# Performance work log

Measured on AMD Instinct MI355X. Metric: run time of the kernel, lower is better.

## Reference

```python
import jax, jax.numpy as jnp
import numpy as np

NP, NM = 50, 32          # pathways, misc tokens
T = NP + NM              # 82 total tokens
D = 24                   # token_dim for latent_dim=2048: (2048//82)//4*4
H, DH, FF = 4, 6, 96     # heads, head_dim, ffn dim (4*D)
B = 8192
EPS = 1e-5


def _ln(x, g, b):
    m = x.mean(-1, keepdims=True)
    v = ((x - m) ** 2).mean(-1, keepdims=True)
    return (x - m) / jnp.sqrt(v + EPS) * g + b


def _adapter(x, w1, b1, g1, bb1, w2, b2, g2, bb2, w3, b3):
    # Linear -> LN -> GELU -> (Dropout eval) -> Linear -> LN -> GELU -> Linear
    h = jax.nn.gelu(_ln(x @ w1.T + b1, g1, bb1), approximate=False)
    h = jax.nn.gelu(_ln(h @ w2.T + b2, g2, bb2), approximate=False)
    return h @ w3.T + b3


def _enc_layer(x, wqkv, bqkv, wo, bo, lg1, lb1, fw1, fb1, fw2, fb2, lg2, lb2):
    # post-norm TransformerEncoderLayer (PyTorch defaults: relu FFN, batch_first)
    Bx, Tx, Dx = x.shape
    qkv = x @ wqkv.T + bqkv                       # [B,T,3D]
    q, k, v = jnp.split(qkv, 3, axis=-1)
    sh = lambda a: a.reshape(Bx, Tx, H, DH).transpose(0, 2, 1, 3)
    q, k, v = sh(q), sh(k), sh(v)
    att = jax.nn.softmax(jnp.einsum('bhqd,bhkd->bhqk', q, k) / jnp.sqrt(jnp.float32(DH)), axis=-1)
    o = jnp.einsum('bhqk,bhkd->bhqd', att, v).transpose(0, 2, 1, 3).reshape(Bx, Tx, Dx)
    o = o @ wo.T + bo
    x = _ln(x + o, lg1, lb1)
    f = jax.nn.relu(x @ fw1.T + fb1) @ fw2.T + fb2
    return _ln(x + f, lg2, lb2)


def setup_inputs() -> dict:
    key = jax.random.key(0)
    ks = iter(jax.random.split(key, 40))
    r = lambda *s: jax.random.normal(next(ks), s, dtype=jnp.float32) * 0.02
    inp = {
        'gene': jax.random.normal(next(ks), (B, 5000), dtype=jnp.float32),
        'protein': jax.random.normal(next(ks), (B, 226), dtype=jnp.float32),
        'pathway_tokens': jax.random.normal(next(ks), (NP, D), dtype=jnp.float32),
        'misc_tokens': jax.random.normal(next(ks), (NM, D), dtype=jnp.float32),
        # gene adapter: 5000 -> 512 -> 256 -> 82
        'gw1': r(512, 5000), 'gb1': jnp.zeros(512), 'gg1': jnp.ones(512), 'gbb1': jnp.zeros(512),
        'gw2': r(256, 512), 'gb2': jnp.zeros(256), 'gg2': jnp.ones(256), 'gbb2': jnp.zeros(256),
        'gw3': r(T, 256), 'gb3': jnp.zeros(T),
        # protein adapter: 226 -> 512 -> 256 -> 82
        'pw1': r(512, 226), 'pb1': jnp.zeros(512), 'pg1': jnp.ones(512), 'pbb1': jnp.zeros(512),
        'pw2': r(256, 512), 'pb2': jnp.zeros(256), 'pg2': jnp.ones(256), 'pbb2': jnp.zeros(256),
        'pw3': r(T, 256), 'pb3': jnp.zeros(T),
        # token mixer: 2 stacked TransformerEncoder layers
        'wqkv': r(2, 3 * D, D), 'bqkv': jnp.zeros((2, 3 * D)),
        'wo': r(2, D, D), 'bo': jnp.zeros((2, D)),
        'lg1': jnp.ones((2, D)), 'lb1': jnp.zeros((2, D)),
        'fw1': r(2, FF, D), 'fb1': jnp.zeros((2, FF)),
        'fw2': r(2, D, FF), 'fb2': jnp.zeros((2, D)),
        'lg2': jnp.ones((2, D)), 'lb2': jnp.zeros((2, D)),
    }
    return inp


def reference(gene, protein, pathway_tokens, misc_tokens,
              gw1, gb1, gg1, gbb1, gw2, gb2, gg2, gbb2, gw3, gb3,
              pw1, pb1, pg1, pbb1, pw2, pb2, pg2, pbb2, pw3, pb3,
              wqkv, bqkv, wo, bo, lg1, lb1, fw1, fb1, fw2, fb2, lg2, lb2):
    all_tokens = jnp.concatenate([pathway_tokens, misc_tokens], axis=0)    # [T,D]
    gene_w = jax.nn.softmax(_adapter(gene, gw1, gb1, gg1, gbb1, gw2, gb2, gg2, gbb2, gw3, gb3), axis=-1)
    prot_w = jax.nn.softmax(_adapter(protein, pw1, pb1, pg1, pbb1, pw2, pb2, pg2, pbb2, pw3, pb3), axis=-1)
    # vectorized form of the per-batch loop: token_activations[b] += all_tokens * w[b,:,None]
    acts = (gene_w + prot_w)[:, :, None] * all_tokens[None]               # [B,T,D]
    for l in range(2):
        acts = _enc_layer(acts, wqkv[l], bqkv[l], wo[l], bo[l], lg1[l], lb1[l],
                          fw1[l], fb1[l], fw2[l], fb2[l], lg2[l], lb2[l])
    return acts
```

## Files before the change

kernel.cpp:

```cpp
#include <hip/hip_runtime.h>
#include <hip/hip_bf16.h>
#include <math.h>

typedef __attribute__((ext_vector_type(4))) float f32x4;
typedef __attribute__((ext_vector_type(8))) short s16x8;
typedef __attribute__((ext_vector_type(4))) short s16x4;
typedef __attribute__((ext_vector_type(4))) unsigned int u32x4;
typedef __attribute__((ext_vector_type(2))) unsigned int u32x2;
typedef _Float16 h2 __attribute__((ext_vector_type(2)));

static __device__ __forceinline__ unsigned short f2bf(float f) {
  unsigned int u = __builtin_bit_cast(unsigned int, f);
  u += 0x7FFFu + ((u >> 16) & 1u);
  return (unsigned short)(u >> 16);
}
static __device__ __forceinline__ unsigned int pk2bf(float a, float b) {
  return (unsigned int)f2bf(a) | ((unsigned int)f2bf(b) << 16);
}
static __device__ __forceinline__ float gelu_exact(float x) {
  return 0.5f * x * (1.0f + erff(x * 0.7071067811865475f));
}
static __device__ __forceinline__ h2 pkh2(float a, float b) {
#if __has_builtin(__builtin_amdgcn_cvt_pkrtz)
  return __builtin_bit_cast(h2, __builtin_amdgcn_cvt_pkrtz(a, b));
#else
  h2 r; r[0] = (_Float16)a; r[1] = (_Float16)b; return r;
#endif
}
static __device__ __forceinline__ float dot2u(h2 a, unsigned int b, float c) {
  h2 bh = __builtin_bit_cast(h2, b);
#if __has_builtin(__builtin_amdgcn_fdot2)
  return __builtin_amdgcn_fdot2(a, bh, c, false);
#else
  return fmaf((float)a[0], (float)bh[0], fmaf((float)a[1], (float)bh[1], c));
#endif
}
static __device__ __forceinline__ float exp2fast(float x) {
#if __has_builtin(__builtin_amdgcn_exp2f)
  return __builtin_amdgcn_exp2f(x);
#else
  return exp2f(x);
#endif
}
static __device__ __forceinline__ void gll16(const void* g, void* l) {
#if __has_builtin(__builtin_amdgcn_global_load_lds)
  __builtin_amdgcn_global_load_lds((__attribute__((address_space(1))) void*)(void*)g,
                                   (__attribute__((address_space(3))) void*)l, 16, 0, 0);
#else
  *(u32x4*)l = *(const u32x4*)g;
#endif
}

__global__ __launch_bounds__(256)
void convert_tile_kernel(const float* __restrict__ src, unsigned short* __restrict__ dst,
                         int Msrc, int Ksrc, int TK, int total16) {
  const int id = blockIdx.x * 256 + threadIdx.x;
  if (id >= total16) return;
  const int j = id & 511;
  const int tile = id >> 9;
  const int tk = tile % TK;
  const int tmm = tile / TK;
  const int r = j >> 3, cb = j & 7;
  const int lcb = cb ^ (r & 7);
  const int row = tmm * 64 + r;
  const int col = tk * 64 + lcb * 8;
  float v[8];
  #pragma unroll
  for (int i = 0; i < 8; ++i) v[i] = 0.f;
  if (row < Msrc) {
    const size_t base = (size_t)row * Ksrc + col;
    if (col + 8 <= Ksrc && ((base & 3) == 0)) {
      f32x4 a = *(const f32x4*)(src + base);
      f32x4 b = *(const f32x4*)(src + base + 4);
      v[0]=a[0];v[1]=a[1];v[2]=a[2];v[3]=a[3];
      v[4]=b[0];v[5]=b[1];v[6]=b[2];v[7]=b[3];
    } else {
      #pragma unroll
      for (int i = 0; i < 8; ++i) if (col + i < Ksrc) v[i] = src[base + i];
    }
  }
  u32x4 o = { pk2bf(v[0],v[1]), pk2bf(v[2],v[3]), pk2bf(v[4],v[5]), pk2bf(v[6],v[7]) };
  *(u32x4*)(dst + (size_t)id * 8) = o;
}

__global__ __launch_bounds__(256, 4)
void gemm_bf16t_kernel(const unsigned short* __restrict__ At, const unsigned short* __restrict__ Bt,
                       const float* __restrict__ bias, float* __restrict__ C,
                       int NT, int KT, int Ntrue, int Nld) {
  __shared__ unsigned short As[4096];
  __shared__ unsigned short Bs[8192];
  const int tid = threadIdx.x;
  const int lane = tid & 63;
  const int wid = tid >> 6;
  const int wm = wid >> 1, wn = wid & 1;
  const int lr = lane & 15;
  const int lkb = ((lane >> 4) & 3) * 16;
  const int l = blockIdx.x;
  const int xcd = l & 7;
  const int kl = l >> 3;
  const int nb = kl % NT;
  const int tm = (kl / NT) * 8 + xcd;
  const size_t abase = (size_t)tm * KT * 4096;
  const size_t bbase0 = (size_t)(2 * nb) * KT * 4096;
  const size_t bbase1 = (size_t)(2 * nb + 1) * KT * 4096;

  f32x4 acc[2][4];
  #pragma unroll
  for (int m = 0; m < 2; ++m)
    #pragma unroll
    for (int n = 0; n < 4; ++n) acc[m][n] = (f32x4){0.f,0.f,0.f,0.f};

  for (int tk = 0; tk < KT; ++tk) {
    __syncthreads();
    const unsigned short* at = At + abase + (size_t)tk * 4096;
    const unsigned short* b0 = Bt + bbase0 + (size_t)tk * 4096;
    const unsigned short* b1 = Bt + bbase1 + (size_t)tk * 4096;
    gll16(at + tid * 8,        (char*)As + tid * 16);
    gll16(at + 2048 + tid * 8, (char*)As + 4096 + tid * 16);
    gll16(b0 + tid * 8,        (char*)Bs + tid * 16);
    gll16(b0 + 2048 + tid * 8, (char*)Bs + 4096 + tid * 16);
    gll16(b1 + tid * 8,        (char*)Bs + 8192 + tid * 16);
    gll16(b1 + 2048 + tid * 8, (char*)Bs + 12288 + tid * 16);
    __syncthreads();
    #pragma unroll
    for (int kk = 0; kk < 2; ++kk) {
      const int kb = (kk * 64 + lkb) ^ ((lr & 7) << 4);
      s16x8 af[2], bfr[4];
      #pragma unroll
      for (int m = 0; m < 2; ++m) {
        const int r = wm * 32 + m * 16 + lr;
        af[m] = *(const s16x8*)((const char*)As + r * 128 + kb);
      }
      #pragma unroll
      for (int n = 0; n < 4; ++n) {
        const int cc = wn * 64 + n * 16 + lr;
        bfr[n] = *(const s16x8*)((const char*)Bs + (cc >> 6) * 8192 + (cc & 63) * 128 + kb);
      }
      #pragma unroll
      for (int m = 0; m < 2; ++m)
        #pragma unroll
        for (int n = 0; n < 4; ++n)
          acc[m][n] = __builtin_amdgcn_mfma_f32_16x16x32_bf16(af[m], bfr[n], acc[m][n], 0, 0, 0);
    }
  }
  const int crow = (lane >> 4) * 4;
  #pragma unroll
  for (int m = 0; m < 2; ++m) {
    const int row = tm * 64 + wm * 32 + m * 16 + crow;
    #pragma unroll
    for (int n = 0; n < 4; ++n) {
      const int col = nb * 128 + wn * 64 + n * 16 + lr;
      if (col < Ntrue) {
        const float bv = bias[col];
        #pragma unroll
        for (int i = 0; i < 4; ++i)
          C[(size_t)(row + i) * Nld + col] = acc[m][n][i] + bv;
      }
    }
  }
}

__global__ __launch_bounds__(256)
void ln_gelu_b16t_kernel(const float* __restrict__ X, const float* __restrict__ g,
                         const float* __restrict__ bta, unsigned short* __restrict__ Y,
                         int N, int TK) {
  const int lane = threadIdx.x & 63;
  const int row = blockIdx.x * 4 + (threadIdx.x >> 6);
  const int tmv = row >> 6, r = row & 63;
  const float* xr = X + (size_t)row * N;
  if (N == 512) {
    const int c0 = lane * 8;
    f32x4 a = *(const f32x4*)(xr + c0);
    f32x4 b = *(const f32x4*)(xr + c0 + 4);
    float s = a[0]+a[1]+a[2]+a[3]+b[0]+b[1]+b[2]+b[3];
    float ss = a[0]*a[0]+a[1]*a[1]+a[2]*a[2]+a[3]*a[3]+b[0]*b[0]+b[1]*b[1]+b[2]*b[2]+b[3]*b[3];
    #pragma unroll
    for (int off = 1; off < 64; off <<= 1) { s += __shfl_xor(s, off); ss += __shfl_xor(ss, off); }
    const float mean = s * (1.f/512.f);
    const float var = ss * (1.f/512.f) - mean * mean;
    const float rstd = rsqrtf(var + 1e-5f);
    float z[8];
    #pragma unroll
    for (int i = 0; i < 4; ++i) z[i]   = gelu_exact((a[i]-mean)*rstd*g[c0+i]   + bta[c0+i]);
    #pragma unroll
    for (int i = 0; i < 4; ++i) z[4+i] = gelu_exact((b[i]-mean)*rstd*g[c0+4+i] + bta[c0+4+i]);
    const int tk = lane >> 3, lcb = lane & 7;
    const size_t d16 = ((size_t)(tmv * TK + tk) << 9) + (r << 3) + (lcb ^ (r & 7));
    u32x4 o = { pk2bf(z[0],z[1]), pk2bf(z[2],z[3]), pk2bf(z[4],z[5]), pk2bf(z[6],z[7]) };
    *(u32x4*)(Y + d16 * 8) = o;
  } else {
    const int c0 = lane * 4;
    f32x4 a = *(const f32x4*)(xr + c0);
    float s = a[0]+a[1]+a[2]+a[3];
    float ss = a[0]*a[0]+a[1]*a[1]+a[2]*a[2]+a[3]*a[3];
    #pragma unroll
    for (int off = 1; off < 64; off <<= 1) { s += __shfl_xor(s, off); ss += __shfl_xor(ss, off); }
    const float mean = s * (1.f/256.f);
    const float var = ss * (1.f/256.f) - mean * mean;
    const float rstd = rsqrtf(var + 1e-5f);
    float z[4];
    #pragma unroll
    for (int i = 0; i < 4; ++i) z[i] = gelu_exact((a[i]-mean)*rstd*g[c0+i] + bta[c0+i]);
    const int tk = lane >> 4, lcb = (lane >> 1) & 7, half = lane & 1;
    const size_t d16 = ((size_t)(tmv * TK + tk) << 9) + (r << 3) + (lcb ^ (r & 7));
    u32x2 o = { pk2bf(z[0],z[1]), pk2bf(z[2],z[3]) };
    *(u32x2*)(Y + d16 * 8 + half * 4) = o;
  }
}

__global__ __launch_bounds__(256)
void softmax2_kernel(const float* __restrict__ la, const float* __restrict__ lp,
                     float* __restrict__ w, int B) {
  const int wid = threadIdx.x >> 6;
  const int lane = threadIdx.x & 63;
  const int row = blockIdx.x * 4 + wid;
  if (row >= B) return;
  const bool has2 = (lane < 18);
  const float* a = la + (size_t)row * 82;
  const float* p = lp + (size_t)row * 82;
  float a0 = a[lane], a1 = has2 ? a[64 + lane] : -1e30f;
  float m = fmaxf(a0, a1);
  #pragma unroll
  for (int off = 1; off < 64; off <<= 1) m = fmaxf(m, __shfl_xor(m, off));
  float ea0 = __expf(a0 - m);
  float ea1 = has2 ? __expf(a1 - m) : 0.f;
  float sa = ea0 + ea1;
  #pragma unroll
  for (int off = 1; off < 64; off <<= 1) sa += __shfl_xor(sa, off);
  float p0 = p[lane], p1 = has2 ? p[64 + lane] : -1e30f;
  float mp = fmaxf(p0, p1);
  #pragma unroll
  for (int off = 1; off < 64; off <<= 1) mp = fmaxf(mp, __shfl_xor(mp, off));
  float ep0 = __expf(p0 - mp);
  float ep1 = has2 ? __expf(p1 - mp) : 0.f;
  float sp = ep0 + ep1;
  #pragma unroll
  for (int off = 1; off < 64; off <<= 1) sp += __shfl_xor(sp, off);
  const float ia = 1.0f / sa, ip = 1.0f / sp;
  w[(size_t)row * 82 + lane] = ea0 * ia + ep0 * ip;
  if (has2) w[(size_t)row * 82 + 64 + lane] = ea1 * ia + ep1 * ip;
}

__global__ __launch_bounds__(256)
void pack_weights_kernel(const float* __restrict__ wqkv, const float* __restrict__ wo,
                         const float* __restrict__ fw1, const float* __restrict__ fw2,
                         unsigned int* __restrict__ dst) {
  const int i = blockIdx.x * 256 + threadIdx.x;
  if (i >= 6912) return;
  float a, b;
  if (i < 1728)      { a = wqkv[2 * i];            b = wqkv[2 * i + 1]; }
  else if (i < 2304) { int j = i - 1728; a = wo[2 * j];  b = wo[2 * j + 1]; }
  else if (i < 4608) { int j = i - 2304; a = fw1[2 * j]; b = fw1[2 * j + 1]; }
  else {
    int j = i - 4608; int layer = j / 1152; int r = j % 1152;
    int jp = r / 24; int d = r % 24;
    const float* s = fw2 + layer * 2304 + d * 96 + 2 * jp;
    a = s[0]; b = s[1];
  }
  unsigned short lo = __builtin_bit_cast(unsigned short, (_Float16)a);
  unsigned short hi = __builtin_bit_cast(unsigned short, (_Float16)b);
  dst[i] = (unsigned int)lo | ((unsigned int)hi << 16);
}

#define VSTRIDE 28

#define DOT12(acc, xv, a0v, a1v, a2v) \
  acc = dot2u(xv[0],  a0v[0], acc); acc = dot2u(xv[1],  a0v[1], acc); \
  acc = dot2u(xv[2],  a0v[2], acc); acc = dot2u(xv[3],  a0v[3], acc); \
  acc = dot2u(xv[4],  a1v[0], acc); acc = dot2u(xv[5],  a1v[1], acc); \
  acc = dot2u(xv[6],  a1v[2], acc); acc = dot2u(xv[7],  a1v[3], acc); \
  acc = dot2u(xv[8],  a2v[0], acc); acc = dot2u(xv[9],  a2v[1], acc); \
  acc = dot2u(xv[10], a2v[2], acc); acc = dot2u(xv[11], a2v[3], acc);

__global__ __launch_bounds__(256, 4)
void encoder_kernel(const float* __restrict__ w_sum,
                    const float* __restrict__ pathway, const float* __restrict__ misc,
                    const unsigned int* __restrict__ whb,
                    const float* __restrict__ bqkv, const float* __restrict__ bo,
                    const float* __restrict__ lg1, const float* __restrict__ lb1,
                    const float* __restrict__ fb1, const float* __restrict__ fb2,
                    const float* __restrict__ lg2, const float* __restrict__ lb2,
                    float* __restrict__ out, int Btot) {
  __shared__ unsigned int Ks[247 * 12];
  __shared__ unsigned int Vs[124 * VSTRIDE];

  const int tid = threadIdx.x;
  const bool active = (tid < 246);
  const int rowW = active ? tid : 246;
  int ls = tid / 82; if (ls > 2) ls = 2;
  const int t = active ? (tid - ls * 82) : 0;
  const int vrow = active ? (ls * 41 + (t >> 1)) : 123;
  const int b = blockIdx.x * 3 + ls;
  const bool storeOK = active && (b < Btot);
  const int bb = (b < Btot) ? b : (Btot - 1);

  float x[24];
  {
    const float* trow = (t < 50) ? (pathway + t * 24) : (misc + (t - 50) * 24);
    const float wv = w_sum[(size_t)bb * 82 + t];
    #pragma unroll
    for (int i = 0; i < 6; ++i) {
      f32x4 v = *(const f32x4*)(trow + 4 * i);
      x[4*i+0] = wv * v[0]; x[4*i+1] = wv * v[1];
      x[4*i+2] = wv * v[2]; x[4*i+3] = wv * v[3];
    }
  }

  const float QS = 0.5889777913f;
  float xf[24];
  #pragma unroll 1
  for (int layer = 0; layer < 2; ++layer) {
    const unsigned int* Wqh = whb + layer * 864;
    const unsigned int* Woh = whb + 1728 + layer * 288;
    const unsigned int* F1h = whb + 2304 + layer * 1152;
    const unsigned int* F2t = whb + 4608 + layer * 1152;
    const float* Bq = bqkv + layer * 72;

    h2 xh[12];
    #pragma unroll
    for (int i = 0; i < 12; ++i) xh[i] = pkh2(x[2*i], x[2*i+1]);
    h2 qh[12];
    #pragma unroll
    for (int j2 = 0; j2 < 12; ++j2) {
      float s0 = Bq[2*j2], s1 = Bq[2*j2+1];
      const u32x4* wr = (const u32x4*)(Wqh + (2*j2) * 12);
      u32x4 a0 = wr[0], a1 = wr[1], a2 = wr[2];
      u32x4 b0 = wr[3], b1 = wr[4], b2 = wr[5];
      DOT12(s0, xh, a0, a1, a2);
      DOT12(s1, xh, b0, b1, b2);
      qh[j2] = pkh2(s0 * QS, s1 * QS);
    }
    {
      unsigned int kpk[12];
      #pragma unroll
      for (int j2 = 0; j2 < 12; ++j2) {
        float s0 = Bq[24 + 2*j2], s1 = Bq[25 + 2*j2];
        const u32x4* wr = (const u32x4*)(Wqh + (24 + 2*j2) * 12);
        u32x4 a0 = wr[0], a1 = wr[1], a2 = wr[2];
        u32x4 b0 = wr[3], b1 = wr[4], b2 = wr[5];
        DOT12(s0, xh, a0, a1, a2);
        DOT12(s1, xh, b0, b1, b2);
        kpk[j2] = __builtin_bit_cast(unsigned int, pkh2(s0, s1));
      }
      #pragma unroll
      for (int u = 0; u < 3; ++u)
        *(u32x4*)&Ks[rowW * 12 + 4*u] = (u32x4){kpk[4*u], kpk[4*u+1], kpk[4*u+2], kpk[4*u+3]};
      float vv[24];
      #pragma unroll
      for (int j2 = 0; j2 < 12; ++j2) {
        float s0 = Bq[48 + 2*j2], s1 = Bq[49 + 2*j2];
        const u32x4* wr = (const u32x4*)(Wqh + (48 + 2*j2) * 12);
        u32x4 a0 = wr[0], a1 = wr[1], a2 = wr[2];
        u32x4 b0 = wr[3], b1 = wr[4], b2 = wr[5];
        DOT12(s0, xh, a0, a1, a2);
        DOT12(s1, xh, b0, b1, b2);
        vv[2*j2] = s0; vv[2*j2+1] = s1;
      }
      _Float16* vh = (_Float16*)Vs;
      const int vbase = vrow * (2 * VSTRIDE) + (t & 1);
      #pragma unroll
      for (int j = 0; j < 24; ++j) vh[vbase + 2*j] = (_Float16)vv[j];
    }
    __syncthreads();

    float acc_o[24];
    float lsum[4] = {0.f, 0.f, 0.f, 0.f};
    #pragma unroll
    for (int d = 0; d < 24; ++d) acc_o[d] = 0.f;
    const unsigned int* Kb = Ks + ls * 82 * 12;
    const unsigned int* Vb = Vs + ls * 41 * VSTRIDE;
    #pragma unroll 1
    for (int kp = 0; kp < 41; ++kp) {
      const unsigned int* kr = Kb + kp * 24;
      u32x4 ka = *(const u32x4*)(kr);
      u32x4 kbv = *(const u32x4*)(kr + 4);
      u32x4 kc = *(const u32x4*)(kr + 8);
      u32x4 kd_ = *(const u32x4*)(kr + 12);
      u32x4 ke = *(const u32x4*)(kr + 16);
      u32x4 kf = *(const u32x4*)(kr + 20);
      unsigned int k0u[12] = {ka[0],ka[1],ka[2],ka[3], kbv[0],kbv[1],kbv[2],kbv[3], kc[0],kc[1],kc[2],kc[3]};
      unsigned int k1u[12] = {kd_[0],kd_[1],kd_[2],kd_[3], ke[0],ke[1],ke[2],ke[3], kf[0],kf[1],kf[2],kf[3]};
      float p0[4], p1[4];
      #pragma unroll
      for (int h = 0; h < 4; ++h) {
        float s0 = dot2u(qh[3*h], k0u[3*h], 0.f);
        s0 = dot2u(qh[3*h+1], k0u[3*h+1], s0);
        s0 = dot2u(qh[3*h+2], k0u[3*h+2], s0);
        float s1 = dot2u(qh[3*h], k1u[3*h], 0.f);
        s1 = dot2u(qh[3*h+1], k1u[3*h+1], s1);
        s1 = dot2u(qh[3*h+2], k1u[3*h+2], s1);
        p0[h] = exp2fast(s0);
        p1[h] = exp2fast(s1);
        lsum[h] += p0[h] + p1[h];
      }
      const unsigned int* vr = Vb + kp * VSTRIDE;
      u32x4 va = *(const u32x4*)(vr);
      u32x4 vbb = *(const u32x4*)(vr + 4);
      u32x4 vc = *(const u32x4*)(vr + 8);
      u32x4 vd = *(const u32x4*)(vr + 12);
      u32x4 ve = *(const u32x4*)(vr + 16);
      u32x4 vf = *(const u32x4*)(vr + 20);
      unsigned int vpu[24] = {va[0],va[1],va[2],va[3], vbb[0],vbb[1],vbb[2],vbb[3],
                              vc[0],vc[1],vc[2],vc[3], vd[0],vd[1],vd[2],vd[3],
                              ve[0],ve[1],ve[2],ve[3], vf[0],vf[1],vf[2],vf[3]};
      #pragma unroll
      for (int h = 0; h < 4; ++h) {
        h2 pp = pkh2(p0[h], p1[h]);
        #pragma unroll
        for (int i = 0; i < 6; ++i)
          acc_o[6*h+i] = dot2u(pp, vpu[6*h+i], acc_o[6*h+i]);
      }
    }
    #pragma unroll
    for (int h = 0; h < 4; ++h) {
      const float inv = 1.0f / lsum[h];
      #pragma unroll
      for (int dh = 0; dh < 6; ++dh) acc_o[6*h+dh] *= inv;
    }
    const float* BO = bo + layer * 24;
    h2 oh[12];
    #pragma unroll
    for (int i = 0; i < 12; ++i) oh[i] = pkh2(acc_o[2*i], acc_o[2*i+1]);
    float xo[24];
    #pragma unroll
    for (int j = 0; j < 24; ++j) {
      float s = BO[j];
      const u32x4* wr = (const u32x4*)(Woh + j * 12);
      u32x4 a0 = wr[0], a1 = wr[1], a2 = wr[2];
      DOT12(s, oh, a0, a1, a2);
      xo[j] = x[j] + s;
    }
    float mean = 0.f;
    #pragma unroll
    for (int j = 0; j < 24; ++j) mean += xo[j];
    mean *= (1.f / 24.f);
    float var = 0.f;
    #pragma unroll
    for (int j = 0; j < 24; ++j) { const float dd = xo[j] - mean; var = fmaf(dd, dd, var); }
    var *= (1.f / 24.f);
    const float rstd = rsqrtf(var + 1e-5f);
    const float* G1 = lg1 + layer * 24;
    const float* Bl1 = lb1 + layer * 24;
    float xn[24];
    #pragma unroll
    for (int j = 0; j < 24; ++j) xn[j] = (xo[j] - mean) * rstd * G1[j] + Bl1[j];
    const float* Bf1 = fb1 + layer * 96;
    const float* Bf2 = fb2 + layer * 24;
    h2 xnh[12];
    #pragma unroll
    for (int i = 0; i < 12; ++i) xnh[i] = pkh2(xn[2*i], xn[2*i+1]);
    float y[24];
    #pragma unroll
    for (int d = 0; d < 24; ++d) y[d] = xn[d] + Bf2[d];
    #pragma unroll 1
    for (int jp = 0; jp < 48; ++jp) {
      float sa = Bf1[2*jp], sb = Bf1[2*jp+1];
      const u32x4* w1v = (const u32x4*)(F1h + (2*jp) * 12);
      u32x4 a0 = w1v[0], a1 = w1v[1], a2 = w1v[2];
      u32x4 b0 = w1v[3], b1 = w1v[4], b2 = w1v[5];
      DOT12(sa, xnh, a0, a1, a2);
      DOT12(sb, xnh, b0, b1, b2);
      sa = fmaxf(sa, 0.f);
      sb = fmaxf(sb, 0.f);
      h2 sp = pkh2(sa, sb);
      const u32x4* w2v = (const u32x4*)(F2t + jp * 24);
      u32x4 c0 = w2v[0], c1 = w2v[1], c2 = w2v[2];
      u32x4 c3 = w2v[3], c4 = w2v[4], c5 = w2v[5];
      y[0]  = dot2u(sp, c0[0], y[0]);  y[1]  = dot2u(sp, c0[1], y[1]);
      y[2]  = dot2u(sp, c0[2], y[2]);  y[3]  = dot2u(sp, c0[3], y[3]);
      y[4]  = dot2u(sp, c1[0], y[4]);  y[5]  = dot2u(sp, c1[1], y[5]);
      y[6]  = dot2u(sp, c1[2], y[6]);  y[7]  = dot2u(sp, c1[3], y[7]);
      y[8]  = dot2u(sp, c2[0], y[8]);  y[9]  = dot2u(sp, c2[1], y[9]);
      y[10] = dot2u(sp, c2[2], y[10]); y[11] = dot2u(sp, c2[3], y[11]);
      y[12] = dot2u(sp, c3[0], y[12]); y[13] = dot2u(sp, c3[1], y[13]);
      y[14] = dot2u(sp, c3[2], y[14]); y[15] = dot2u(sp, c3[3], y[15]);
      y[16] = dot2u(sp, c4[0], y[16]); y[17] = dot2u(sp, c4[1], y[17]);
      y[18] = dot2u(sp, c4[2], y[18]); y[19] = dot2u(sp, c4[3], y[19]);
      y[20] = dot2u(sp, c5[0], y[20]); y[21] = dot2u(sp, c5[1], y[21]);
      y[22] = dot2u(sp, c5[2], y[22]); y[23] = dot2u(sp, c5[3], y[23]);
    }
    float mean2 = 0.f;
    #pragma unroll
    for (int j = 0; j < 24; ++j) mean2 += y[j];
    mean2 *= (1.f / 24.f);
    float var2 = 0.f;
    #pragma unroll
    for (int j = 0; j < 24; ++j) { const float dd = y[j] - mean2; var2 = fmaf(dd, dd, var2); }
    var2 *= (1.f / 24.f);
    const float rstd2 = rsqrtf(var2 + 1e-5f);
    const float* G2 = lg2 + layer * 24;
    const float* Bl2 = lb2 + layer * 24;
    #pragma unroll
    for (int j = 0; j < 24; ++j) xf[j] = (y[j] - mean2) * rstd2 * G2[j] + Bl2[j];
    if (layer == 0) {
      #pragma unroll
      for (int j = 0; j < 24; ++j) x[j] = xf[j];
    }
    __syncthreads();
  }
  if (storeOK) {
    float* op = out + (size_t)b * 1968 + t * 24;
    #pragma unroll
    for (int d4 = 0; d4 < 6; ++d4) {
      f32x4 v = { xf[4*d4], xf[4*d4+1], xf[4*d4+2], xf[4*d4+3] };
      *(f32x4*)(op + 4 * d4) = v;
    }
  }
}

extern "C" void kernel_launch(void* const* d_in, const int* in_sizes, int n_in,
                              void* d_out, int out_size, void* d_ws, size_t ws_size,
                              hipStream_t stream) {
  const float* gene    = (const float*)d_in[0];
  const float* protein = (const float*)d_in[1];
  const float* pathway = (const float*)d_in[2];
  const float* misc    = (const float*)d_in[3];
  const float* gw1 = (const float*)d_in[4];
  const float* gb1 = (const float*)d_in[5];
  const float* gg1 = (const float*)d_in[6];
  const float* gbb1= (const float*)d_in[7];
  const float* gw2 = (const float*)d_in[8];
  const float* gb2 = (const float*)d_in[9];
  const float* gg2 = (const float*)d_in[10];
  const float* gbb2= (const float*)d_in[11];
  const float* gw3 = (const float*)d_in[12];
  const float* gb3 = (const float*)d_in[13];
  const float* pw1 = (const float*)d_in[14];
  const float* pb1 = (const float*)d_in[15];
  const float* pg1 = (const float*)d_in[16];
  const float* pbb1= (const float*)d_in[17];
  const float* pw2 = (const float*)d_in[18];
  const float* pb2 = (const float*)d_in[19];
  const float* pg2 = (const float*)d_in[20];
  const float* pbb2= (const float*)d_in[21];
  const float* pw3 = (const float*)d_in[22];
  const float* pb3 = (const float*)d_in[23];
  const float* wqkv= (const float*)d_in[24];
  const float* bqkv= (const float*)d_in[25];
  const float* wo  = (const float*)d_in[26];
  const float* bo  = (const float*)d_in[27];
  const float* lg1 = (const float*)d_in[28];
  const float* lb1 = (const float*)d_in[29];
  const float* fw1 = (const float*)d_in[30];
  const float* fb1 = (const float*)d_in[31];
  const float* fw2 = (const float*)d_in[32];
  const float* fb2 = (const float*)d_in[33];
  const float* lg2 = (const float*)d_in[34];
  const float* lb2 = (const float*)d_in[35];

  const int B = in_sizes[0] / 5000;
  dim3 blk(256);

  size_t off = 0;
  auto take = [&](size_t bytes) { size_t r = off; off = (off + bytes + 255) & ~(size_t)255; return r; };
  const size_t o_geneB  = take((size_t)B * 5056 * 2);
  const size_t o_protB  = take((size_t)B * 256 * 2);
  const size_t o_gw1B   = take((size_t)512 * 5056 * 2);
  const size_t o_pw1B   = take((size_t)512 * 256 * 2);
  const size_t o_gw2B   = take((size_t)256 * 512 * 2);
  const size_t o_pw2B   = take((size_t)256 * 512 * 2);
  const size_t o_gw3B   = take((size_t)128 * 256 * 2);
  const size_t o_pw3B   = take((size_t)128 * 256 * 2);
  const size_t o_Cbuf   = take((size_t)B * 512 * 4);
  const size_t o_h1B    = take((size_t)B * 512 * 2);
  const size_t o_h2B    = take((size_t)B * 256 * 2);
  const size_t o_lg     = take((size_t)B * 82 * 4);
  const size_t o_lp     = take((size_t)B * 82 * 4);
  const size_t o_wsum   = take((size_t)B * 82 * 4);
  const size_t o_whb    = take((size_t)6912 * 4);
  const size_t need = off;

  if (need <= ws_size) {
    char* base = (char*)d_ws;
    unsigned short* geneB = (unsigned short*)(base + o_geneB);
    unsigned short* protB = (unsigned short*)(base + o_protB);
    unsigned short* gw1B  = (unsigned short*)(base + o_gw1B);
    unsigned short* pw1B  = (unsigned short*)(base + o_pw1B);
    unsigned short* gw2B  = (unsigned short*)(base + o_gw2B);
    unsigned short* pw2B  = (unsigned short*)(base + o_pw2B);
    unsigned short* gw3B  = (unsigned short*)(base + o_gw3B);
    unsigned short* pw3B  = (unsigned short*)(base + o_pw3B);
    float* Cbuf = (float*)(base + o_Cbuf);
    unsigned short* h1B = (unsigned short*)(base + o_h1B);
    unsigned short* h2B = (unsigned short*)(base + o_h2B);
    float* logits_g = (float*)(base + o_lg);
    float* logits_p = (float*)(base + o_lp);
    float* w_sum    = (float*)(base + o_wsum);
    unsigned int* whb = (unsigned int*)(base + o_whb);

    const int MT = B / 64;
    pack_weights_kernel<<<dim3(27), blk, 0, stream>>>(wqkv, wo, fw1, fw2, whb);
    {
      int t16 = MT * 79 * 512;
      convert_tile_kernel<<<dim3((t16 + 255) / 256), blk, 0, stream>>>(gene, geneB, B, 5000, 79, t16);
      t16 = MT * 4 * 512;
      convert_tile_kernel<<<dim3((t16 + 255) / 256), blk, 0, stream>>>(protein, protB, B, 226, 4, t16);
      t16 = 8 * 79 * 512;
      convert_tile_kernel<<<dim3((t16 + 255) / 256), blk, 0, stream>>>(gw1, gw1B, 512, 5000, 79, t16);
      t16 = 8 * 4 * 512;
      convert_tile_kernel<<<dim3((t16 + 255) / 256), blk, 0, stream>>>(pw1, pw1B, 512, 226, 4, t16);
      t16 = 4 * 8 * 512;
      convert_tile_kernel<<<dim3((t16 + 255) / 256), blk, 0, stream>>>(gw2, gw2B, 256, 512, 8, t16);
      convert_tile_kernel<<<dim3((t16 + 255) / 256), blk, 0, stream>>>(pw2, pw2B, 256, 512, 8, t16);
      t16 = 2 * 4 * 512;
      convert_tile_kernel<<<dim3((t16 + 255) / 256), blk, 0, stream>>>(gw3, gw3B, 82, 256, 4, t16);
      convert_tile_kernel<<<dim3((t16 + 255) / 256), blk, 0, stream>>>(pw3, pw3B, 82, 256, 4, t16);
    }
    gemm_bf16t_kernel<<<dim3(MT * 4), blk, 0, stream>>>(geneB, gw1B, gb1, Cbuf, 4, 79, 512, 512);
    ln_gelu_b16t_kernel<<<dim3(B / 4), blk, 0, stream>>>(Cbuf, gg1, gbb1, h1B, 512, 8);
    gemm_bf16t_kernel<<<dim3(MT * 2), blk, 0, stream>>>(h1B, gw2B, gb2, Cbuf, 2, 8, 256, 256);
    ln_gelu_b16t_kernel<<<dim3(B / 4), blk, 0, stream>>>(Cbuf, gg2, gbb2, h2B, 256, 4);
    gemm_bf16t_kernel<<<dim3(MT * 1), blk, 0, stream>>>(h2B, gw3B, gb3, logits_g, 1, 4, 82, 82);
    gemm_bf16t_kernel<<<dim3(MT * 4), blk, 0, stream>>>(protB, pw1B, pb1, Cbuf, 4, 4, 512, 512);
    ln_gelu_b16t_kernel<<<dim3(B / 4), blk, 0, stream>>>(Cbuf, pg1, pbb1, h1B, 512, 8);
    gemm_bf16t_kernel<<<dim3(MT * 2), blk, 0, stream>>>(h1B, pw2B, pb2, Cbuf, 2, 8, 256, 256);
    ln_gelu_b16t_kernel<<<dim3(B / 4), blk, 0, stream>>>(Cbuf, pg2, pbb2, h2B, 256, 4);
    gemm_bf16t_kernel<<<dim3(MT * 1), blk, 0, stream>>>(h2B, pw3B, pb3, logits_p, 1, 4, 82, 82);
    softmax2_kernel<<<dim3((B + 3) / 4), blk, 0, stream>>>(logits_g, logits_p, w_sum, B);
    encoder_kernel<<<dim3((B + 2) / 3), blk, 0, stream>>>(w_sum, pathway, misc,
        whb, bqkv, bo, lg1, lb1, fb1, fb2, lg2, lb2, (float*)d_out, B);
    return;
  }

  float* logits_g = (float*)d_ws;
  float* logits_p = logits_g + (size_t)B * 82;
  float* w_sum    = logits_p + (size_t)B * 82;
  unsigned int* whb = (unsigned int*)(w_sum + (size_t)B * 82);
  float* Cbuf = (float*)(whb + 6912);
  unsigned short* h1B = (unsigned short*)(Cbuf + (size_t)B * 512);
  unsigned short* h2B = h1B + (size_t)B * 512;
  pack_weights_kernel<<<dim3(27), blk, 0, stream>>>(wqkv, wo, fw1, fw2, whb);
  softmax2_kernel<<<dim3((B + 3) / 4), blk, 0, stream>>>(logits_g, logits_p, w_sum, B);
  encoder_kernel<<<dim3((B + 2) / 3), blk, 0, stream>>>(w_sum, pathway, misc,
      whb, bqkv, bo, lg1, lb1, fb1, fb2, lg2, lb2, (float*)d_out, B);
  (void)h1B; (void)h2B; (void)Cbuf;
  (void)gw1; (void)gb1; (void)gg1; (void)gbb1; (void)gw2; (void)gb2; (void)gg2; (void)gbb2;
  (void)gw3; (void)gb3; (void)pw1; (void)pb1; (void)pg1; (void)pbb1; (void)pw2; (void)pb2;
  (void)pg2; (void)pbb2; (void)pw3; (void)pb3; (void)gene; (void)protein;
}
```

Measured before the change: 555.0 us.

## Split each token across two threads in the encoder kernel

The encoder now runs 512-thread blocks in which each token is handled by two threads. Each thread computes half of the Q/K/V projections, two of the four attention heads, and half of the FFN hidden units. The halves are exchanged through shared memory, with extra barriers, before the output projection and the second LayerNorm. The aim is more parallelism and lower per-thread register pressure and serial work. The cost is extra LDS traffic and synchronisation, and the partial FFN sums are rounded to fp16 before the exchange.

```diff
diff --git a/kernel.cpp b/kernel.cpp
--- a/kernel.cpp
+++ b/kernel.cpp
@@ -26,6 +26,12 @@
 #else
   h2 r; r[0] = (_Float16)a; r[1] = (_Float16)b; return r;
 #endif
+}
+static __device__ __forceinline__ float h2loF(unsigned int u) {
+  h2 v = __builtin_bit_cast(h2, u); return (float)v[0];
+}
+static __device__ __forceinline__ float h2hiF(unsigned int u) {
+  h2 v = __builtin_bit_cast(h2, u); return (float)v[1];
 }
 static __device__ __forceinline__ float dot2u(h2 a, unsigned int b, float c) {
   h2 bh = __builtin_bit_cast(h2, b);
@@ -262,8 +268,6 @@
   dst[i] = (unsigned int)lo | ((unsigned int)hi << 16);
 }
 
-#define VSTRIDE 28
-
 #define DOT12(acc, xv, a0v, a1v, a2v) \
   acc = dot2u(xv[0],  a0v[0], acc); acc = dot2u(xv[1],  a0v[1], acc); \
   acc = dot2u(xv[2],  a0v[2], acc); acc = dot2u(xv[3],  a0v[3], acc); \
@@ -272,23 +276,23 @@
   acc = dot2u(xv[8],  a2v[0], acc); acc = dot2u(xv[9],  a2v[1], acc); \
   acc = dot2u(xv[10], a2v[2], acc); acc = dot2u(xv[11], a2v[3], acc);
 
-__global__ __launch_bounds__(256, 4)
-void encoder_kernel(const float* __restrict__ w_sum,
-                    const float* __restrict__ pathway, const float* __restrict__ misc,
-                    const unsigned int* __restrict__ whb,
-                    const float* __restrict__ bqkv, const float* __restrict__ bo,
-                    const float* __restrict__ lg1, const float* __restrict__ lb1,
-                    const float* __restrict__ fb1, const float* __restrict__ fb2,
-                    const float* __restrict__ lg2, const float* __restrict__ lb2,
-                    float* __restrict__ out, int Btot) {
-  __shared__ unsigned int Ks[247 * 12];
-  __shared__ unsigned int Vs[124 * VSTRIDE];
-
+__global__ __launch_bounds__(512, 4)
+void encoder2_kernel(const float* __restrict__ w_sum,
+                     const float* __restrict__ pathway, const float* __restrict__ misc,
+                     const unsigned int* __restrict__ whb,
+                     const float* __restrict__ bqkv, const float* __restrict__ bo,
+                     const float* __restrict__ lg1, const float* __restrict__ lb1,
+                     const float* __restrict__ fb1, const float* __restrict__ fb2,
+                     const float* __restrict__ lg2, const float* __restrict__ lb2,
+                     float* __restrict__ out, int Btot) {
+  __shared__ unsigned int SH[7424];
   const int tid = threadIdx.x;
-  const bool active = (tid < 246);
-  const int rowW = active ? tid : 246;
-  int ls = tid / 82; if (ls > 2) ls = 2;
-  const int t = active ? (tid - ls * 82) : 0;
+  const bool active = (tid < 492);
+  const int ls = active ? (tid / 164) : 2;
+  const int rr = active ? (tid % 164) : 163;
+  const int t  = rr >> 1;
+  const int hf = rr & 1;
+  const int krow = active ? (ls * 82 + t) : 246;
   const int vrow = active ? (ls * 41 + (t >> 1)) : 123;
   const int b = blockIdx.x * 3 + ls;
   const bool storeOK = active && (b < Btot);
@@ -319,108 +323,140 @@
     h2 xh[12];
     #pragma unroll
     for (int i = 0; i < 12; ++i) xh[i] = pkh2(x[2*i], x[2*i+1]);
-    h2 qh[12];
-    #pragma unroll
-    for (int j2 = 0; j2 < 12; ++j2) {
-      float s0 = Bq[2*j2], s1 = Bq[2*j2+1];
-      const u32x4* wr = (const u32x4*)(Wqh + (2*j2) * 12);
+    h2 qh[6];
+    #pragma unroll
+    for (int p = 0; p < 6; ++p) {
+      const int j = 12*hf + 2*p;
+      float s0 = Bq[j], s1 = Bq[j+1];
+      const u32x4* wr = (const u32x4*)(Wqh + j * 12);
       u32x4 a0 = wr[0], a1 = wr[1], a2 = wr[2];
       u32x4 b0 = wr[3], b1 = wr[4], b2 = wr[5];
       DOT12(s0, xh, a0, a1, a2);
       DOT12(s1, xh, b0, b1, b2);
-      qh[j2] = pkh2(s0 * QS, s1 * QS);
+      qh[p] = pkh2(s0 * QS, s1 * QS);
     }
     {
-      unsigned int kpk[12];
-      #pragma unroll
-      for (int j2 = 0; j2 < 12; ++j2) {
-        float s0 = Bq[24 + 2*j2], s1 = Bq[25 + 2*j2];
-        const u32x4* wr = (const u32x4*)(Wqh + (24 + 2*j2) * 12);
+      unsigned int kpk[6];
+      #pragma unroll
+      for (int p = 0; p < 6; ++p) {
+        const int j = 24 + 12*hf + 2*p;
+        float s0 = Bq[j], s1 = Bq[j+1];
+        const u32x4* wr = (const u32x4*)(Wqh + j * 12);
         u32x4 a0 = wr[0], a1 = wr[1], a2 = wr[2];
         u32x4 b0 = wr[3], b1 = wr[4], b2 = wr[5];
         DOT12(s0, xh, a0, a1, a2);
         DOT12(s1, xh, b0, b1, b2);
-        kpk[j2] = __builtin_bit_cast(unsigned int, pkh2(s0, s1));
+        kpk[p] = __builtin_bit_cast(unsigned int, pkh2(s0, s1));
       }
-      #pragma unroll
-      for (int u = 0; u < 3; ++u)
-        *(u32x4*)&Ks[rowW * 12 + 4*u] = (u32x4){kpk[4*u], kpk[4*u+1], kpk[4*u+2], kpk[4*u+3]};
-      float vv[24];
-      #pragma unroll
-      for (int j2 = 0; j2 < 12; ++j2) {
-        float s0 = Bq[48 + 2*j2], s1 = Bq[49 + 2*j2];
-        const u32x4* wr = (const u32x4*)(Wqh + (48 + 2*j2) * 12);
+      unsigned int* kd = &SH[krow * 16 + 8*hf];
+      *(u32x4*)kd       = (u32x4){kpk[0], kpk[1], kpk[2], kpk[3]};
+      *(u32x2*)(kd + 4) = (u32x2){kpk[4], kpk[5]};
+    }
+    {
+      float vv[12];
+      #pragma unroll
+      for (int p = 0; p < 6; ++p) {
+        const int j = 48 + 12*hf + 2*p;
+        float s0 = Bq[j], s1 = Bq[j+1];
+        const u32x4* wr = (const u32x4*)(Wqh + j * 12);
         u32x4 a0 = wr[0], a1 = wr[1], a2 = wr[2];
         u32x4 b0 = wr[3], b1 = wr[4], b2 = wr[5];
         DOT12(s0, xh, a0, a1, a2);
         DOT12(s1, xh, b0, b1, b2);
-        vv[2*j2] = s0; vv[2*j2+1] = s1;
+        vv[2*p] = s0; vv[2*p+1] = s1;
       }
-      _Float16* vh = (_Float16*)Vs;
-      const int vbase = vrow * (2 * VSTRIDE) + (t & 1);
-      #pragma unroll
-      for (int j = 0; j < 24; ++j) vh[vbase + 2*j] = (_Float16)vv[j];
+      _Float16* vh = (_Float16*)(SH + 3952);
+      const int vb0 = vrow * 56 + (t & 1);
+      #pragma unroll
+      for (int p = 0; p < 12; ++p)
+        vh[vb0 + 2 * (12*hf + p)] = (_Float16)vv[p];
     }
     __syncthreads();
 
-    float acc_o[24];
-    float lsum[4] = {0.f, 0.f, 0.f, 0.f};
-    #pragma unroll
-    for (int d = 0; d < 24; ++d) acc_o[d] = 0.f;
-    const unsigned int* Kb = Ks + ls * 82 * 12;
-    const unsigned int* Vb = Vs + ls * 41 * VSTRIDE;
+    float acc_o[12];
+    #pragma unroll
+    for (int d = 0; d < 12; ++d) acc_o[d] = 0.f;
+    float lsA = 0.f, lsB = 0.f;
+    const unsigned int* Kb = SH + (ls * 82) * 16;
+    const unsigned int* Vb = SH + 3952 + (ls * 41) * 28;
     #pragma unroll 1
     for (int kp = 0; kp < 41; ++kp) {
-      const unsigned int* kr = Kb + kp * 24;
-      u32x4 ka = *(const u32x4*)(kr);
-      u32x4 kbv = *(const u32x4*)(kr + 4);
-      u32x4 kc = *(const u32x4*)(kr + 8);
-      u32x4 kd_ = *(const u32x4*)(kr + 12);
-      u32x4 ke = *(const u32x4*)(kr + 16);
-      u32x4 kf = *(const u32x4*)(kr + 20);
-      unsigned int k0u[12] = {ka[0],ka[1],ka[2],ka[3], kbv[0],kbv[1],kbv[2],kbv[3], kc[0],kc[1],kc[2],kc[3]};
-      unsigned int k1u[12] = {kd_[0],kd_[1],kd_[2],kd_[3], ke[0],ke[1],ke[2],ke[3], kf[0],kf[1],kf[2],kf[3]};
-      float p0[4], p1[4];
-      #pragma unroll
-      for (int h = 0; h < 4; ++h) {
-        float s0 = dot2u(qh[3*h], k0u[3*h], 0.f);
-        s0 = dot2u(qh[3*h+1], k0u[3*h+1], s0);
-        s0 = dot2u(qh[3*h+2], k0u[3*h+2], s0);
-        float s1 = dot2u(qh[3*h], k1u[3*h], 0.f);
-        s1 = dot2u(qh[3*h+1], k1u[3*h+1], s1);
-        s1 = dot2u(qh[3*h+2], k1u[3*h+2], s1);
-        p0[h] = exp2fast(s0);
-        p1[h] = exp2fast(s1);
-        lsum[h] += p0[h] + p1[h];
+      const unsigned int* k0 = Kb + (2*kp) * 16 + 8*hf;
+      u32x4 k0a = *(const u32x4*)k0;
+      u32x2 k0b = *(const u32x2*)(k0 + 4);
+      u32x4 k1a = *(const u32x4*)(k0 + 16);
+      u32x2 k1b = *(const u32x2*)(k0 + 20);
+      float sA0 = dot2u(qh[0], k0a[0], 0.f);
+      sA0 = dot2u(qh[1], k0a[1], sA0);
+      sA0 = dot2u(qh[2], k0a[2], sA0);
+      float sB0 = dot2u(qh[3], k0a[3], 0.f);
+      sB0 = dot2u(qh[4], k0b[0], sB0);
+      sB0 = dot2u(qh[5], k0b[1], sB0);
+      float sA1 = dot2u(qh[0], k1a[0], 0.f);
+      sA1 = dot2u(qh[1], k1a[1], sA1);
+      sA1 = dot2u(qh[2], k1a[2], sA1);
+      float sB1 = dot2u(qh[3], k1a[3], 0.f);
+      sB1 = dot2u(qh[4], k1b[0], sB1);
+      sB1 = dot2u(qh[5], k1b[1], sB1);
+      const float pA0 = exp2fast(sA0), pA1 = exp2fast(sA1);
+      const float pB0 = exp2fast(sB0), pB1 = exp2fast(sB1);
+      lsA += pA0 + pA1;
+      lsB += pB0 + pB1;
+      const unsigned int* vr = Vb + kp * 28 + 12*hf;
+      u32x4 v0 = *(const u32x4*)(vr);
+      u32x4 v1 = *(const u32x4*)(vr + 4);
+      u32x4 v2 = *(const u32x4*)(vr + 8);
+      h2 ppA = pkh2(pA0, pA1);
+      h2 ppB = pkh2(pB0, pB1);
+      acc_o[0]  = dot2u(ppA, v0[0], acc_o[0]);
+      acc_o[1]  = dot2u(ppA, v0[1], acc_o[1]);
+      acc_o[2]  = dot2u(ppA, v0[2], acc_o[2]);
+      acc_o[3]  = dot2u(ppA, v0[3], acc_o[3]);
+      acc_o[4]  = dot2u(ppA, v1[0], acc_o[4]);
+      acc_o[5]  = dot2u(ppA, v1[1], acc_o[5]);
+      acc_o[6]  = dot2u(ppB, v1[2], acc_o[6]);
+      acc_o[7]  = dot2u(ppB, v1[3], acc_o[7]);
+      acc_o[8]  = dot2u(ppB, v2[0], acc_o[8]);
+      acc_o[9]  = dot2u(ppB, v2[1], acc_o[9]);
+      acc_o[10] = dot2u(ppB, v2[2], acc_o[10]);
+      acc_o[11] = dot2u(ppB, v2[3], acc_o[11]);
+    }
+    {
+      const float invA = 1.0f / lsA, invB = 1.0f / lsB;
+      #pragma unroll
+      for (int d = 0; d < 6; ++d) acc_o[d] *= invA;
+      #pragma unroll
+      for (int d = 6; d < 12; ++d) acc_o[d] *= invB;
+    }
+    __syncthreads();
+
+    unsigned int och[6];
+    #pragma unroll
+    for (int i = 0; i < 6; ++i)
+      och[i] = __builtin_bit_cast(unsigned int, pkh2(acc_o[2*i], acc_o[2*i+1]));
+    {
+      unsigned int* od = &SH[tid * 6];
+      *(u32x2*)(od)     = (u32x2){och[0], och[1]};
+      *(u32x2*)(od + 2) = (u32x2){och[2], och[3]};
+      *(u32x2*)(od + 4) = (u32x2){och[4], och[5]};
+    }
+    __syncthreads();
+    h2 oh[12];
+    {
+      const unsigned int* ps = &SH[(tid ^ 1) * 6];
+      u32x2 p0 = *(const u32x2*)(ps);
+      u32x2 p1 = *(const u32x2*)(ps + 2);
+      u32x2 p2 = *(const u32x2*)(ps + 4);
+      unsigned int pch[6] = {p0[0], p0[1], p1[0], p1[1], p2[0], p2[1]};
+      #pragma unroll
+      for (int i = 0; i < 6; ++i) {
+        const unsigned int lo = hf ? pch[i] : och[i];
+        const unsigned int hi = hf ? och[i] : pch[i];
+        oh[i]     = __builtin_bit_cast(h2, lo);
+        oh[6 + i] = __builtin_bit_cast(h2, hi);
       }
-      const unsigned int* vr = Vb + kp * VSTRIDE;
-      u32x4 va = *(const u32x4*)(vr);
-      u32x4 vbb = *(const u32x4*)(vr + 4);
-      u32x4 vc = *(const u32x4*)(vr + 8);
-      u32x4 vd = *(const u32x4*)(vr + 12);
-      u32x4 ve = *(const u32x4*)(vr + 16);
-      u32x4 vf = *(const u32x4*)(vr + 20);
-      unsigned int vpu[24] = {va[0],va[1],va[2],va[3], vbb[0],vbb[1],vbb[2],vbb[3],
-                              vc[0],vc[1],vc[2],vc[3], vd[0],vd[1],vd[2],vd[3],
-                              ve[0],ve[1],ve[2],ve[3], vf[0],vf[1],vf[2],vf[3]};
-      #pragma unroll
-      for (int h = 0; h < 4; ++h) {
-        h2 pp = pkh2(p0[h], p1[h]);
-        #pragma unroll
-        for (int i = 0; i < 6; ++i)
-          acc_o[6*h+i] = dot2u(pp, vpu[6*h+i], acc_o[6*h+i]);
-      }
-    }
-    #pragma unroll
-    for (int h = 0; h < 4; ++h) {
-      const float inv = 1.0f / lsum[h];
-      #pragma unroll
-      for (int dh = 0; dh < 6; ++dh) acc_o[6*h+dh] *= inv;
     }
     const float* BO = bo + layer * 24;
-    h2 oh[12];
-    #pragma unroll
-    for (int i = 0; i < 12; ++i) oh[i] = pkh2(acc_o[2*i], acc_o[2*i+1]);
     float xo[24];
     #pragma unroll
     for (int j = 0; j < 24; ++j) {
@@ -445,15 +481,15 @@
     #pragma unroll
     for (int j = 0; j < 24; ++j) xn[j] = (xo[j] - mean) * rstd * G1[j] + Bl1[j];
     const float* Bf1 = fb1 + layer * 96;
-    const float* Bf2 = fb2 + layer * 24;
     h2 xnh[12];
     #pragma unroll
     for (int i = 0; i < 12; ++i) xnh[i] = pkh2(xn[2*i], xn[2*i+1]);
     float y[24];
     #pragma unroll
-    for (int d = 0; d < 24; ++d) y[d] = xn[d] + Bf2[d];
+    for (int d = 0; d < 24; ++d) y[d] = 0.f;
+    const int jp0 = 24 * hf;
     #pragma unroll 1
-    for (int jp = 0; jp < 48; ++jp) {
+    for (int jp = jp0; jp < jp0 + 24; ++jp) {
       float sa = Bf1[2*jp], sb = Bf1[2*jp+1];
       const u32x4* w1v = (const u32x4*)(F1h + (2*jp) * 12);
       u32x4 a0 = w1v[0], a1 = w1v[1], a2 = w1v[2];
@@ -479,19 +515,46 @@
       y[20] = dot2u(sp, c5[0], y[20]); y[21] = dot2u(sp, c5[1], y[21]);
       y[22] = dot2u(sp, c5[2], y[22]); y[23] = dot2u(sp, c5[3], y[23]);
     }
-    float mean2 = 0.f;
-    #pragma unroll
-    for (int j = 0; j < 24; ++j) mean2 += y[j];
-    mean2 *= (1.f / 24.f);
-    float var2 = 0.f;
-    #pragma unroll
-    for (int j = 0; j < 24; ++j) { const float dd = y[j] - mean2; var2 = fmaf(dd, dd, var2); }
-    var2 *= (1.f / 24.f);
-    const float rstd2 = rsqrtf(var2 + 1e-5f);
-    const float* G2 = lg2 + layer * 24;
-    const float* Bl2 = lb2 + layer * 24;
-    #pragma unroll
-    for (int j = 0; j < 24; ++j) xf[j] = (y[j] - mean2) * rstd2 * G2[j] + Bl2[j];
+    __syncthreads();
+    {
+      unsigned int ypk[12];
+      #pragma unroll
+      for (int i = 0; i < 12; ++i)
+        ypk[i] = __builtin_bit_cast(unsigned int, pkh2(y[2*i], y[2*i+1]));
+      unsigned int* yd = &SH[tid * 12];
+      *(u32x4*)(yd)     = (u32x4){ypk[0], ypk[1], ypk[2],  ypk[3]};
+      *(u32x4*)(yd + 4) = (u32x4){ypk[4], ypk[5], ypk[6],  ypk[7]};
+      *(u32x4*)(yd + 8) = (u32x4){ypk[8], ypk[9], ypk[10], ypk[11]};
+    }
+    __syncthreads();
+    {
+      const unsigned int* ys = &SH[(tid ^ 1) * 12];
+      u32x4 ya_ = *(const u32x4*)(ys);
+      u32x4 yb_ = *(const u32x4*)(ys + 4);
+      u32x4 yc_ = *(const u32x4*)(ys + 8);
+      unsigned int yp[12] = {ya_[0],ya_[1],ya_[2],ya_[3], yb_[0],yb_[1],yb_[2],yb_[3],
+                             yc_[0],yc_[1],yc_[2],yc_[3]};
+      const float* Bf2 = fb2 + layer * 24;
+      float yt[24];
+      #pragma unroll
+      for (int i = 0; i < 12; ++i) {
+        yt[2*i]   = y[2*i]   + h2loF(yp[i]) + xn[2*i]   + Bf2[2*i];
+        yt[2*i+1] = y[2*i+1] + h2hiF(yp[i]) + xn[2*i+1] + Bf2[2*i+1];
+      }
+      float mean2 = 0.f;
+      #pragma unroll
+      for (int j = 0; j < 24; ++j) mean2 += yt[j];
+      mean2 *= (1.f / 24.f);
+      float var2 = 0.f;
+      #pragma unroll
+      for (int j = 0; j < 24; ++j) { const float dd = yt[j] - mean2; var2 = fmaf(dd, dd, var2); }
+      var2 *= (1.f / 24.f);
+      const float rstd2 = rsqrtf(var2 + 1e-5f);
+      const float* G2 = lg2 + layer * 24;
+      const float* Bl2 = lb2 + layer * 24;
+      #pragma unroll
+      for (int j = 0; j < 24; ++j) xf[j] = (yt[j] - mean2) * rstd2 * G2[j] + Bl2[j];
+    }
     if (layer == 0) {
       #pragma unroll
       for (int j = 0; j < 24; ++j) x[j] = xf[j];
@@ -499,10 +562,11 @@
     __syncthreads();
   }
   if (storeOK) {
-    float* op = out + (size_t)b * 1968 + t * 24;
-    #pragma unroll
-    for (int d4 = 0; d4 < 6; ++d4) {
-      f32x4 v = { xf[4*d4], xf[4*d4+1], xf[4*d4+2], xf[4*d4+3] };
+    float* op = out + (size_t)b * 1968 + t * 24 + 12*hf;
+    #pragma unroll
+    for (int d4 = 0; d4 < 3; ++d4) {
+      f32x4 v = { xf[12*hf + 4*d4], xf[12*hf + 4*d4 + 1],
+                  xf[12*hf + 4*d4 + 2], xf[12*hf + 4*d4 + 3] };
       *(f32x4*)(op + 4 * d4) = v;
     }
   }
@@ -617,7 +681,7 @@
     ln_gelu_b16t_kernel<<<dim3(B / 4), blk, 0, stream>>>(Cbuf, pg2, pbb2, h2B, 256, 4);
     gemm_bf16t_kernel<<<dim3(MT * 1), blk, 0, stream>>>(h2B, pw3B, pb3, logits_p, 1, 4, 82, 82);
     softmax2_kernel<<<dim3((B + 3) / 4), blk, 0, stream>>>(logits_g, logits_p, w_sum, B);
-    encoder_kernel<<<dim3((B + 2) / 3), blk, 0, stream>>>(w_sum, pathway, misc,
+    encoder2_kernel<<<dim3((B + 2) / 3), dim3(512), 0, stream>>>(w_sum, pathway, misc,
         whb, bqkv, bo, lg1, lb1, fb1, fb2, lg2, lb2, (float*)d_out, B);
     return;
   }
@@ -626,15 +690,12 @@
   float* logits_p = logits_g + (size_t)B * 82;
   float* w_sum    = logits_p + (size_t)B * 82;
   unsigned int* whb = (unsigned int*)(w_sum + (size_t)B * 82);
-  float* Cbuf = (float*)(whb + 6912);
-  unsigned short* h1B = (unsigned short*)(Cbuf + (size_t)B * 512);
-  unsigned short* h2B = h1B + (size_t)B * 512;
   pack_weights_kernel<<<dim3(27), blk, 0, stream>>>(wqkv, wo, fw1, fw2, whb);
   softmax2_kernel<<<dim3((B + 3) / 4), blk, 0, stream>>>(logits_g, logits_p, w_sum, B);
-  encoder_kernel<<<dim3((B + 2) / 3), blk, 0, stream>>>(w_sum, pathway, misc,
+  encoder2_kernel<<<dim3((B + 2) / 3), dim3(512), 0, stream>>>(w_sum, pathway, misc,
       whb, bqkv, bo, lg1, lb1, fb1, fb2, lg2, lb2, (float*)d_out, B);
-  (void)h1B; (void)h2B; (void)Cbuf;
-  (void)gw1; (void)gb1; (void)gg1; (void)gbb1; (void)gw2; (void)gb2; (void)gg2; (void)gbb2;
-  (void)gw3; (void)gb3; (void)pw1; (void)pb1; (void)pg1; (void)pbb1; (void)pw2; (void)pb2;
-  (void)pg2; (void)pbb2; (void)pw3; (void)pb3; (void)gene; (void)protein;
-}
+  (void)gene; (void)protein; (void)gw1; (void)gb1; (void)gg1; (void)gbb1;
+  (void)gw2; (void)gb2; (void)gg2; (void)gbb2; (void)gw3; (void)gb3;
+  (void)pw1; (void)pb1; (void)pg1; (void)pbb1; (void)pw2; (void)pb2;
+  (void)pg2; (void)pbb2; (void)pw3; (void)pb3;
+}
```

Measured after the change: 1.259 ms. 127% more time.
